# Performance work log

Measured on AMD Instinct MI355X. Metric: run time of the kernel, lower is better.

The kernel has to match this reference:

```python
import jax, jax.numpy as jnp
import numpy as np

N_QUBITS = 8
NUM_HEADS = 2
EPS = 1e-5
TWO_PI = 6.283185307179586


def _rx(state, wire, theta, n):
    # state: (B, 2**n) complex64; theta: (B,) float. PennyLane wire 0 = MSB.
    B = state.shape[0]
    st = state.reshape(B, 2 ** wire, 2, 2 ** (n - 1 - wire))
    c = jnp.cos(theta * 0.5).astype(state.dtype)[:, None, None]
    s = ((-1j) * jnp.sin(theta * 0.5).astype(state.dtype))[:, None, None]
    a0 = st[:, :, 0, :]
    a1 = st[:, :, 1, :]
    return jnp.stack([c * a0 + s * a1, s * a0 + c * a1], axis=2).reshape(B, -1)


def _cnot(state, ctrl, tgt, n):
    B = state.shape[0]
    st = state.reshape((B,) + (2,) * n)
    ax_c = ctrl + 1
    ax_t = tgt + 1
    s0 = jnp.take(st, 0, axis=ax_c)
    s1 = jnp.take(st, 1, axis=ax_c)
    ft = ax_t - 1 if ax_t > ax_c else ax_t
    s1 = jnp.flip(s1, axis=ft)
    return jnp.stack([s0, s1], axis=ax_c).reshape(B, -1)


def _vqc(x, weights):
    # AngleEmbedding (RX) + BasicEntanglerLayers (RX per wire + CNOT ring) -> <Z_i>.
    # x: (B, n) angles; weights: (L, n). Returns (B, n) real expvals.
    B, n = x.shape
    state = jnp.zeros((B, 2 ** n), dtype=jnp.complex64).at[:, 0].set(1.0)
    for w in range(n):
        state = _rx(state, w, x[:, w], n)
    pairs = [(i, (i + 1) % n) for i in range(n)] if n > 2 else ([(0, 1)] if n == 2 else [])
    for l in range(weights.shape[0]):
        for w in range(n):
            state = _rx(state, w, jnp.broadcast_to(weights[l, w], (B,)), n)
        for cw, tw in pairs:
            state = _cnot(state, cw, tw, n)
    probs = (state.real ** 2 + state.imag ** 2).reshape((B,) + (2,) * n)
    zs = []
    for w in range(n):
        axes = tuple(a for a in range(1, n + 1) if a != w + 1)
        p = jnp.sum(probs, axis=axes)  # (B, 2)
        zs.append(p[:, 0] - p[:, 1])
    return jnp.stack(zs, axis=-1)


def _layernorm(x, g, b):
    m = jnp.mean(x, axis=-1, keepdims=True)
    v = jnp.mean((x - m) ** 2, axis=-1, keepdims=True)
    return (x - m) / jnp.sqrt(v + EPS) * g + b


def setup_inputs() -> dict:
    key = jax.random.key(0)
    ks = jax.random.split(key, 10)
    E = N_QUBITS
    x = jax.random.normal(ks[0], (64, 256, E), dtype=jnp.float32)
    # TorchLayer default init: uniform(0, 2*pi)
    Wq = jax.random.uniform(ks[1], (1, E), dtype=jnp.float32) * TWO_PI
    Wk = jax.random.uniform(ks[2], (1, E), dtype=jnp.float32) * TWO_PI
    Wv = jax.random.uniform(ks[3], (1, E), dtype=jnp.float32) * TWO_PI
    Wc = jax.random.uniform(ks[4], (1, E), dtype=jnp.float32) * TWO_PI
    Wf = jax.random.uniform(ks[5], (1, E), dtype=jnp.float32) * TWO_PI
    w1 = jax.random.normal(ks[6], (E, E), dtype=jnp.float32) * 0.3
    b1 = jax.random.normal(ks[7], (E,), dtype=jnp.float32) * 0.05
    w2 = jax.random.normal(ks[8], (E, E), dtype=jnp.float32) * 0.3
    b2 = jax.random.normal(ks[9], (E,), dtype=jnp.float32) * 0.05
    gamma1 = jnp.ones((E,), dtype=jnp.float32)
    beta1 = jnp.zeros((E,), dtype=jnp.float32)
    gamma2 = jnp.ones((E,), dtype=jnp.float32)
    beta2 = jnp.zeros((E,), dtype=jnp.float32)
    return {"x": x, "Wq": Wq, "Wk": Wk, "Wv": Wv, "Wc": Wc, "Wf": Wf,
            "w1": w1, "b1": b1, "w2": w2, "b2": b2,
            "gamma1": gamma1, "beta1": beta1, "gamma2": gamma2, "beta2": beta2}


def reference(x, Wq, Wk, Wv, Wc, Wf, w1, b1, w2, b2, gamma1, beta1, gamma2, beta2):
    B, S, E = x.shape
    H = NUM_HEADS
    dk = E // H
    tok = x.reshape(B * S, E)
    Q = _vqc(tok, Wq).reshape(B, S, E)
    K = _vqc(tok, Wk).reshape(B, S, E)
    V = _vqc(tok, Wv).reshape(B, S, E)
    split = lambda t: t.reshape(B, S, H, dk).transpose(0, 2, 1, 3)
    scores = jnp.einsum('bhqd,bhkd->bhqk', split(Q), split(K)) / jnp.sqrt(jnp.float32(dk))
    attn = jax.nn.softmax(scores, axis=-1)  # dropout = identity in eval
    ctx = jnp.einsum('bhqk,bhkd->bhqd', attn, split(V)).transpose(0, 2, 1, 3).reshape(B, S, E)
    attn_out = _vqc(ctx.reshape(B * S, E), Wc).reshape(B, S, E)
    x = _layernorm(x + attn_out, gamma1, beta1)
    h = x @ w1.T + b1                       # linear1 (no activation in FeedForwardQuantum)
    hq = _vqc(h.reshape(B * S, -1), Wf).reshape(B, S, -1)
    ff = hq @ w2.T + b2                     # linear2
    x = _layernorm(x + ff, gamma2, beta2)
    return x
```

## Files before the change

### kernel.cpp

```cpp
#include <hip/hip_runtime.h>


#define SEQ 256
#define EMB 8

static __device__ __forceinline__ void load8f(const float* __restrict__ p, float v[8]) {
    float4 a = *reinterpret_cast<const float4*>(p);
    float4 b = *reinterpret_cast<const float4*>(p + 4);
    v[0] = a.x; v[1] = a.y; v[2] = a.z; v[3] = a.w;
    v[4] = b.x; v[5] = b.y; v[6] = b.z; v[7] = b.w;
}

static __device__ __forceinline__ void store8f(float* __restrict__ p, const float v[8]) {
    *reinterpret_cast<float4*>(p)     = make_float4(v[0], v[1], v[2], v[3]);
    *reinterpret_cast<float4*>(p + 4) = make_float4(v[4], v[5], v[6], v[7]);
}

static __device__ __forceinline__ void vqc8(const float in[8], const float W[8], float z[8]) {
    float c[8];
#pragma unroll
    for (int i = 0; i < 8; ++i) c[i] = __cosf(in[i] + W[i]);
    float t = c[1];
#pragma unroll
    for (int i = 2; i < 8; ++i) t *= c[i];
    z[0] = t;
    float acc = c[0];
#pragma unroll
    for (int i = 1; i < 8; ++i) { acc *= c[i]; z[i] = acc; }
}

static __device__ __forceinline__ void ln8(const float r[8], const float g[8], const float be[8], float o[8]) {
    float m = 0.f;
#pragma unroll
    for (int i = 0; i < 8; ++i) m += r[i];
    m *= 0.125f;
    float var = 0.f;
#pragma unroll
    for (int i = 0; i < 8; ++i) { float d = r[i] - m; var += d * d; }
    var *= 0.125f;
    float inv = rsqrtf(var + 1e-5f);
#pragma unroll
    for (int i = 0; i < 8; ++i) o[i] = (r[i] - m) * inv * g[i] + be[i];
}

__global__ __launch_bounds__(512) void vitq_kernel(
    const float* __restrict__ x,
    const float* __restrict__ Wq, const float* __restrict__ Wk,
    const float* __restrict__ Wv, const float* __restrict__ Wc,
    const float* __restrict__ Wf,
    const float* __restrict__ w1, const float* __restrict__ b1,
    const float* __restrict__ w2, const float* __restrict__ b2,
    const float* __restrict__ g1, const float* __restrict__ be1,
    const float* __restrict__ g2, const float* __restrict__ be2,
    float* __restrict__ out)
{
    __shared__ float Ks[SEQ][EMB];
    __shared__ float Vs[SEQ][EMB];
    __shared__ float Cs[SEQ][EMB];

    const int b   = blockIdx.x;
    const int tid = threadIdx.x;
    const int s   = tid & (SEQ - 1);
    const int h   = tid >> 8;

    float xv[8];
    load8f(x + ((size_t)(b * SEQ + s)) * EMB, xv);

    float wrow[8], q[8];
    load8f(Wq, wrow);
    vqc8(xv, wrow, q);
    if (h == 0) {
        float k[8];
        load8f(Wk, wrow);
        vqc8(xv, wrow, k);
#pragma unroll
        for (int i = 0; i < 8; ++i) Ks[s][i] = k[i];
    } else {
        float v[8];
        load8f(Wv, wrow);
        vqc8(xv, wrow, v);
#pragma unroll
        for (int i = 0; i < 8; ++i) Vs[s][i] = v[i];
    }
    __syncthreads();

    const int ho = 4 * h;
    float qh[4];
#pragma unroll
    for (int d = 0; d < 4; ++d) qh[d] = q[ho + d] * 0.5f;

    float l = 0.f;
    float acc0 = 0.f, acc1 = 0.f, acc2 = 0.f, acc3 = 0.f;
#pragma unroll 8
    for (int kk = 0; kk < SEQ; ++kk) {
        float4 kr = *reinterpret_cast<const float4*>(&Ks[kk][ho]);
        float4 vr = *reinterpret_cast<const float4*>(&Vs[kk][ho]);
        float sc = qh[0] * kr.x + qh[1] * kr.y + qh[2] * kr.z + qh[3] * kr.w;
        float e  = __expf(sc);
        l    += e;
        acc0 += e * vr.x;
        acc1 += e * vr.y;
        acc2 += e * vr.z;
        acc3 += e * vr.w;
    }
    float inv = 1.f / l;
    Cs[s][ho + 0] = acc0 * inv;
    Cs[s][ho + 1] = acc1 * inv;
    Cs[s][ho + 2] = acc2 * inv;
    Cs[s][ho + 3] = acc3 * inv;
    __syncthreads();

    if (h == 0) {
        float ctx[8];
#pragma unroll
        for (int i = 0; i < 8; ++i) ctx[i] = Cs[s][i];

        float ao[8];
        load8f(Wc, wrow);
        vqc8(ctx, wrow, ao);

        float r[8];
#pragma unroll
        for (int i = 0; i < 8; ++i) r[i] = xv[i] + ao[i];

        float g[8], be[8], x1[8];
        load8f(g1, g); load8f(be1, be);
        ln8(r, g, be, x1);

        float wf[64], bias[8];
#pragma unroll
        for (int i = 0; i < 64; ++i) wf[i] = w1[i];
        load8f(b1, bias);
        float hv[8];
#pragma unroll
        for (int j = 0; j < 8; ++j) {
            float a = bias[j];
#pragma unroll
            for (int i = 0; i < 8; ++i) a += x1[i] * wf[j * 8 + i];
            hv[j] = a;
        }

        float hq[8];
        load8f(Wf, wrow);
        vqc8(hv, wrow, hq);

#pragma unroll
        for (int i = 0; i < 64; ++i) wf[i] = w2[i];
        load8f(b2, bias);
        float r2[8];
#pragma unroll
        for (int j = 0; j < 8; ++j) {
            float a = bias[j];
#pragma unroll
            for (int i = 0; i < 8; ++i) a += hq[i] * wf[j * 8 + i];
            r2[j] = x1[j] + a;
        }

        float o[8];
        load8f(g2, g); load8f(be2, be);
        ln8(r2, g, be, o);

        store8f(out + ((size_t)(b * SEQ + s)) * EMB, o);
    }
}

extern "C" void kernel_launch(void* const* d_in, const int* in_sizes, int n_in,
                              void* d_out, int out_size, void* d_ws, size_t ws_size,
                              hipStream_t stream) {
    const float* x   = (const float*)d_in[0];
    const float* Wq  = (const float*)d_in[1];
    const float* Wk  = (const float*)d_in[2];
    const float* Wv  = (const float*)d_in[3];
    const float* Wc  = (const float*)d_in[4];
    const float* Wf  = (const float*)d_in[5];
    const float* w1  = (const float*)d_in[6];
    const float* b1  = (const float*)d_in[7];
    const float* w2  = (const float*)d_in[8];
    const float* b2  = (const float*)d_in[9];
    const float* g1  = (const float*)d_in[10];
    const float* be1 = (const float*)d_in[11];
    const float* g2  = (const float*)d_in[12];
    const float* be2 = (const float*)d_in[13];
    float* out = (float*)d_out;

    const int B = in_sizes[0] / (SEQ * EMB);
    vitq_kernel<<<B, 512, 0, stream>>>(x, Wq, Wk, Wv, Wc, Wf, w1, b1, w2, b2,
                                       g1, be1, g2, be2, out);
}
```

Baseline: 96.52 us.

## Split attention across query groups and key chunks to launch more blocks

```diff
diff --git a/kernel.cpp b/kernel.cpp
--- a/kernel.cpp
+++ b/kernel.cpp
@@ -3,6 +3,8 @@
 
 #define SEQ 256
 #define EMB 8
+#define QG  64
+#define NSPLIT 4
 
 static __device__ __forceinline__ void load8f(const float* __restrict__ p, float v[8]) {
     float4 a = *reinterpret_cast<const float4*>(p);
@@ -56,31 +58,38 @@
 {
     __shared__ float Ks[SEQ][EMB];
     __shared__ float Vs[SEQ][EMB];
-    __shared__ float Cs[SEQ][EMB];
-
-    const int b   = blockIdx.x;
+    __shared__ float P[NSPLIT][2 * QG][5];
+
+    const int bi  = blockIdx.x;
+    const int b   = bi >> 2;
+    const int g   = bi & 3;
     const int tid = threadIdx.x;
-    const int s   = tid & (SEQ - 1);
-    const int h   = tid >> 8;
-
-    float xv[8];
-    load8f(x + ((size_t)(b * SEQ + s)) * EMB, xv);
-
-    float wrow[8], q[8];
+    const int p   = tid & 127;
+    const int j   = tid >> 7;
+    const int sl  = p & 63;
+    const int h   = p >> 6;
+    const int s   = g * QG + sl;
+
+    const float* xb = x + ((size_t)b * SEQ) * EMB;
+
+    float xq[8], wrow[8], q[8];
+    load8f(xb + (size_t)s * EMB, xq);
     load8f(Wq, wrow);
-    vqc8(xv, wrow, q);
-    if (h == 0) {
-        float k[8];
-        load8f(Wk, wrow);
-        vqc8(xv, wrow, k);
-#pragma unroll
-        for (int i = 0; i < 8; ++i) Ks[s][i] = k[i];
-    } else {
-        float v[8];
-        load8f(Wv, wrow);
-        vqc8(xv, wrow, v);
-#pragma unroll
-        for (int i = 0; i < 8; ++i) Vs[s][i] = v[i];
+    vqc8(xq, wrow, q);
+
+    {
+        const int t = tid & 255;
+        float xs[8], kv[8];
+        load8f(xb + (size_t)t * EMB, xs);
+        if (tid < 256) {
+            load8f(Wk, wrow);
+            vqc8(xs, wrow, kv);
+            store8f(&Ks[t][0], kv);
+        } else {
+            load8f(Wv, wrow);
+            vqc8(xs, wrow, kv);
+            store8f(&Vs[t][0], kv);
+        }
     }
     __syncthreads();
 
@@ -89,10 +98,10 @@
 #pragma unroll
     for (int d = 0; d < 4; ++d) qh[d] = q[ho + d] * 0.5f;
 
-    float l = 0.f;
-    float acc0 = 0.f, acc1 = 0.f, acc2 = 0.f, acc3 = 0.f;
+    float l = 0.f, acc0 = 0.f, acc1 = 0.f, acc2 = 0.f, acc3 = 0.f;
+    const int k0 = j * 64;
 #pragma unroll 8
-    for (int kk = 0; kk < SEQ; ++kk) {
+    for (int kk = k0; kk < k0 + 64; ++kk) {
         float4 kr = *reinterpret_cast<const float4*>(&Ks[kk][ho]);
         float4 vr = *reinterpret_cast<const float4*>(&Vs[kk][ho]);
         float sc = qh[0] * kr.x + qh[1] * kr.y + qh[2] * kr.z + qh[3] * kr.w;
@@ -103,17 +112,33 @@
         acc2 += e * vr.z;
         acc3 += e * vr.w;
     }
-    float inv = 1.f / l;
-    Cs[s][ho + 0] = acc0 * inv;
-    Cs[s][ho + 1] = acc1 * inv;
-    Cs[s][ho + 2] = acc2 * inv;
-    Cs[s][ho + 3] = acc3 * inv;
+    P[j][p][0] = l;
+    P[j][p][1] = acc0;
+    P[j][p][2] = acc1;
+    P[j][p][3] = acc2;
+    P[j][p][4] = acc3;
     __syncthreads();
 
-    if (h == 0) {
+    if (tid < QG) {
         float ctx[8];
 #pragma unroll
-        for (int i = 0; i < 8; ++i) ctx[i] = Cs[s][i];
+        for (int hh = 0; hh < 2; ++hh) {
+            const int pp = hh * QG + tid;
+            float ll = 0.f, a0 = 0.f, a1 = 0.f, a2 = 0.f, a3 = 0.f;
+#pragma unroll
+            for (int jj = 0; jj < NSPLIT; ++jj) {
+                ll += P[jj][pp][0];
+                a0 += P[jj][pp][1];
+                a1 += P[jj][pp][2];
+                a2 += P[jj][pp][3];
+                a3 += P[jj][pp][4];
+            }
+            float inv = 1.f / ll;
+            ctx[4 * hh + 0] = a0 * inv;
+            ctx[4 * hh + 1] = a1 * inv;
+            ctx[4 * hh + 2] = a2 * inv;
+            ctx[4 * hh + 3] = a3 * inv;
+        }
 
         float ao[8];
         load8f(Wc, wrow);
@@ -121,11 +146,11 @@
 
         float r[8];
 #pragma unroll
-        for (int i = 0; i < 8; ++i) r[i] = xv[i] + ao[i];
-
-        float g[8], be[8], x1[8];
-        load8f(g1, g); load8f(be1, be);
-        ln8(r, g, be, x1);
+        for (int i = 0; i < 8; ++i) r[i] = xq[i] + ao[i];
+
+        float gg[8], be[8], x1[8];
+        load8f(g1, gg); load8f(be1, be);
+        ln8(r, gg, be, x1);
 
         float wf[64], bias[8];
 #pragma unroll
@@ -133,11 +158,11 @@
         load8f(b1, bias);
         float hv[8];
 #pragma unroll
-        for (int j = 0; j < 8; ++j) {
-            float a = bias[j];
-#pragma unroll
-            for (int i = 0; i < 8; ++i) a += x1[i] * wf[j * 8 + i];
-            hv[j] = a;
+        for (int jj = 0; jj < 8; ++jj) {
+            float a = bias[jj];
+#pragma unroll
+            for (int i = 0; i < 8; ++i) a += x1[i] * wf[jj * 8 + i];
+            hv[jj] = a;
         }
 
         float hq[8];
@@ -149,16 +174,16 @@
         load8f(b2, bias);
         float r2[8];
 #pragma unroll
-        for (int j = 0; j < 8; ++j) {
-            float a = bias[j];
-#pragma unroll
-            for (int i = 0; i < 8; ++i) a += hq[i] * wf[j * 8 + i];
-            r2[j] = x1[j] + a;
+        for (int jj = 0; jj < 8; ++jj) {
+            float a = bias[jj];
+#pragma unroll
+            for (int i = 0; i < 8; ++i) a += hq[i] * wf[jj * 8 + i];
+            r2[jj] = x1[jj] + a;
         }
 
         float o[8];
-        load8f(g2, g); load8f(be2, be);
-        ln8(r2, g, be, o);
+        load8f(g2, gg); load8f(be2, be);
+        ln8(r2, gg, be, o);
 
         store8f(out + ((size_t)(b * SEQ + s)) * EMB, o);
     }
@@ -184,6 +209,6 @@
     float* out = (float*)d_out;
 
     const int B = in_sizes[0] / (SEQ * EMB);
-    vitq_kernel<<<B, 512, 0, stream>>>(x, Wq, Wk, Wv, Wc, Wf, w1, b1, w2, b2,
-                                       g1, be1, g2, be2, out);
-}
+    vitq_kernel<<<B * 4, 512, 0, stream>>>(x, Wq, Wk, Wv, Wc, Wf, w1, b1, w2, b2,
+                                           g1, be1, g2, be2, out);
+}
```

Result: faster. 86.93 us (-9.9%).
